# Optimization experiments

Hardware: AMD Instinct MI355X
Metric: run time of the kernel (lower is better)

The kernel has to match this reference:

```python
import jax, jax.numpy as jnp
import numpy as np


def setup_inputs() -> dict:
    key = jax.random.key(0)
    ks = jax.random.split(key, 5)
    B, S, D = 2, 2048, 1024
    x = jax.random.normal(ks[0], (B, S, D), dtype=jnp.float32)
    # nn.Linear default init scale ~ 1/sqrt(fan_in); use scaled normals
    W_qkv = jax.random.normal(ks[1], (3 * D, D), dtype=jnp.float32) * (1.0 / np.sqrt(D))
    b_qkv = jax.random.normal(ks[2], (3 * D,), dtype=jnp.float32) * 0.01
    W_out = jax.random.normal(ks[3], (D, D), dtype=jnp.float32) * (1.0 / np.sqrt(D))
    b_out = jax.random.normal(ks[4], (D,), dtype=jnp.float32) * 0.01
    return {"x": x, "W_qkv": W_qkv, "b_qkv": b_qkv, "W_out": W_out, "b_out": b_out, "n_heads": 16}


def reference(x, W_qkv, b_qkv, W_out, b_out, n_heads):
    B, S, D = x.shape
    H = n_heads
    c = D // H
    scale = jnp.asarray(1.0 / np.sqrt(c), dtype=x.dtype)
    # qkv projection; torch layout: (head, qkv, c) along the 3*D output dim
    qkv = (x @ W_qkv.T + b_qkv).reshape(B, S, H, 3, c)
    q = qkv[..., 0, :]  # (B, S, H, c)
    k = qkv[..., 1, :]
    v = qkv[..., 2, :]
    scores = jnp.einsum("bshd,bthd->bhst", q, k) * scale  # (B, H, S, S)
    # mask='right': forbid attending to future positions (col > row)
    causal = jnp.arange(S)[None, :] > jnp.arange(S)[:, None]  # (S, S) True where future
    scores = jnp.where(causal[None, None], -jnp.inf, scores)
    attn = jax.nn.softmax(scores, axis=-1)
    ctx = jnp.einsum("bhst,bthd->bshd", attn, v).reshape(B, S, D)
    return ctx @ W_out.T + b_out
```

## Files before the change

kernel.cpp:

```cpp
#include <hip/hip_runtime.h>
#include <stdint.h>

#define B_ 2
#define S_ 2048
#define D_ 1024
#define H_ 16
#define C_ 64
#define M_ (B_*S_)
#define N1_ (3*D_)

typedef float f32x4 __attribute__((ext_vector_type(4)));
typedef float f32x16 __attribute__((ext_vector_type(16)));
typedef __bf16 bf16x8 __attribute__((ext_vector_type(8)));

#define QSCALE 0.18033688f

static __device__ __forceinline__ unsigned short f2bf(float f) {
  __bf16 h = (__bf16)f;
  return __builtin_bit_cast(unsigned short, h);
}
static __device__ __forceinline__ unsigned pk2(float lo, float hi) {
  return (unsigned)f2bf(lo) | ((unsigned)f2bf(hi) << 16);
}

static __device__ __forceinline__ f32x4 mfma_bf16(uint4 a, uint4 b, f32x4 c) {
  return __builtin_amdgcn_mfma_f32_16x16x32_bf16(
      __builtin_bit_cast(bf16x8, a), __builtin_bit_cast(bf16x8, b), c, 0, 0, 0);
}
static __device__ __forceinline__ f32x16 mfma32(uint4 a, uint4 b, f32x16 c) {
  return __builtin_amdgcn_mfma_f32_32x32x16_bf16(
      __builtin_bit_cast(bf16x8, a), __builtin_bit_cast(bf16x8, b), c, 0, 0, 0);
}

static __device__ __forceinline__ float xsum32(float x) {
  return x + __shfl_xor(x, 32);
}

static __device__ __forceinline__ void gload16(const void* g, void* l) {
  __builtin_amdgcn_global_load_lds(
      (const __attribute__((address_space(1))) unsigned int*)g,
      (__attribute__((address_space(3))) unsigned int*)l, 16, 0, 0);
}

#define N8X (M_*D_/8)
#define N8W (N1_*D_/8)
#define N8O (D_*D_/8)
__global__ __launch_bounds__(256) void cast_all(
    const float* __restrict__ x,   unsigned short* __restrict__ xb,
    const float* __restrict__ wq,  unsigned short* __restrict__ wqb,
    const float* __restrict__ wo,  unsigned short* __restrict__ wob) {
  int i = blockIdx.x * 256 + threadIdx.x;
  const float* src; unsigned short* dst; int j;
  if (i < N8X)              { src = x;  dst = xb;  j = i; }
  else if (i < N8X + N8W)   { src = wq; dst = wqb; j = i - N8X; }
  else                      { src = wo; dst = wob; j = i - N8X - N8W; }
  const float4* s4 = (const float4*)src;
  float4 a = s4[2*j], b = s4[2*j+1];
  uint4 o;
  o.x = pk2(a.x, a.y);
  o.y = pk2(a.z, a.w);
  o.z = pk2(b.x, b.y);
  o.w = pk2(b.z, b.w);
  ((uint4*)dst)[j] = o;
}

template<int MODE>
__global__ __launch_bounds__(256) void gemm_bt(
    const unsigned short* __restrict__ A,
    const unsigned short* __restrict__ Bm,
    const float* __restrict__ bias,
    float* __restrict__ Cf,
    unsigned short* __restrict__ Qg,
    unsigned short* __restrict__ Kf,
    unsigned short* __restrict__ Vf,
    int Ndim, int Kdim)
{
  __shared__ __attribute__((aligned(16))) unsigned short As[128*32];
  __shared__ __attribute__((aligned(16))) unsigned short Bs[128*32];
  const int tid = threadIdx.x;
  const int l = tid & 63, wid = tid >> 6;
  const int g = l >> 4, lr = l & 15;
  const int m0 = blockIdx.y * 128, n0 = blockIdx.x * 128;
  const int wr = (wid >> 1) * 64, wc = (wid & 1) * 64;

  f32x4 acc[4][4] = {};

  const int lane4 = l >> 2;
  const int p4 = l & 3;
  const int cA = p4 ^ (lane4 & 3);
  const int rA = wid*32 + lane4;
  const unsigned short* Agl = A + (size_t)(m0 + rA) * Kdim + cA*8;
  const unsigned short* Bgl = Bm + (size_t)(n0 + rA) * Kdim + cA*8;
  unsigned short* Al0 = &As[(wid*32)*32];
  unsigned short* Al1 = &As[(wid*32+16)*32];
  unsigned short* Bl0 = &Bs[(wid*32)*32];
  unsigned short* Bl1 = &Bs[(wid*32+16)*32];
  const size_t rowstep = (size_t)16 * Kdim;

  for (int k0 = 0; k0 < Kdim; k0 += 32) {
    __syncthreads();
    gload16(Agl + k0,           Al0);
    gload16(Agl + k0 + rowstep, Al1);
    gload16(Bgl + k0,           Bl0);
    gload16(Bgl + k0 + rowstep, Bl1);
    __syncthreads();
    uint4 af[4], bf[4];
#pragma unroll
    for (int mi = 0; mi < 4; ++mi)
      af[mi] = *(const uint4*)&As[(wr + mi*16 + lr)*32 + ((g ^ (lr & 3))*8)];
#pragma unroll
    for (int ni = 0; ni < 4; ++ni)
      bf[ni] = *(const uint4*)&Bs[(wc + ni*16 + lr)*32 + ((g ^ (lr & 3))*8)];
#pragma unroll
    for (int mi = 0; mi < 4; ++mi)
#pragma unroll
      for (int ni = 0; ni < 4; ++ni)
        acc[mi][ni] = mfma_bf16(af[mi], bf[ni], acc[mi][ni]);
  }

#pragma unroll
  for (int mi = 0; mi < 4; ++mi)
#pragma unroll
    for (int ni = 0; ni < 4; ++ni) {
      if (MODE == 0) {
#pragma unroll
        for (int r = 0; r < 4; ++r) {
          const int row = m0 + wr + mi*16 + g*4 + r;
          const int col = n0 + wc + ni*16 + lr;
          Cf[(size_t)row * Ndim + col] = acc[mi][ni][r] + bias[col];
        }
      } else {
        const int colbase = n0 + wc + ni*16;
        const int h     = colbase / 192;
        const int rem   = colbase % 192;
        const int which = rem >> 6;
        const int cb    = rem & 63;
        const float bv  = bias[colbase + lr];
        const int row0  = m0 + wr + mi*16 + g*4;
        const int b     = row0 >> 11, s0 = row0 & 2047;
        const size_t bh32 = (size_t)(b*H_ + h) * 32;
        if (which == 0) {
#pragma unroll
          for (int r = 0; r < 4; ++r) {
            const float v = (acc[mi][ni][r] + bv) * QSCALE;
            Qg[((size_t)(b*H_ + h)*S_ + (s0 + r))*C_ + cb + lr] = f2bf(v);
          }
        } else if (which == 1) {
          const int kc = cb >> 4, hi = lr >> 3, j = lr & 7;
          const int kvb = s0 >> 6, kq = s0 & 63;
          const int half = kq >> 5, qlb = kq & 31;
          const size_t base = (((bh32 + kvb)*2 + half)*4 + kc)*512 + hi*256 + j;
#pragma unroll
          for (int r = 0; r < 4; ++r)
            Kf[base + (size_t)(qlb + r)*8] = f2bf(acc[mi][ni][r] + bv);
        } else {
          const int d = cb + lr;
          const int dhalf = d >> 5, ql = d & 31;
          const int kvb = s0 >> 6, kq = s0 & 63;
          const int kc = kq >> 4, hi = (kq >> 3) & 1, j0 = kq & 7;
          const size_t base = (((bh32 + kvb)*2 + dhalf)*4 + kc)*512
                              + (hi*32 + ql)*8 + j0;
          ushort4 pk;
          pk.x = f2bf(acc[mi][ni][0] + bv);
          pk.y = f2bf(acc[mi][ni][1] + bv);
          pk.z = f2bf(acc[mi][ni][2] + bv);
          pk.w = f2bf(acc[mi][ni][3] + bv);
          *(ushort4*)(Vf + base) = pk;
        }
      }
    }
}

#define PS_ 72
__global__ __launch_bounds__(256) void attn_fwd(
    const unsigned short* __restrict__ Qg,
    const unsigned short* __restrict__ Kf,
    const unsigned short* __restrict__ Vf,
    unsigned short* __restrict__ ctx)
{
  __shared__ __attribute__((aligned(16))) unsigned short Ps[4][32*PS_];

  const int tid = threadIdx.x, l = tid & 63, w = tid >> 6;
  const int ql = l & 31, hi = l >> 5;
  const int bh = blockIdx.x;
  const int y = (int)blockIdx.y;
  const int qtab[4] = {y, 63 - y, 31 - y, 32 + y};
  const int qt = qtab[w];
  const int qw0 = qt * 32;
  const int qg = qw0 + ql;
  const size_t baseK = (size_t)bh * S_ * C_;

  uint4 qreg[4];
  {
    const unsigned short* qp = Qg + baseK + (size_t)qg * C_ + hi * 8;
#pragma unroll
    for (int kc = 0; kc < 4; ++kc) qreg[kc] = *(const uint4*)(qp + 16*kc);
  }

  f32x16 acc0 = {}, acc1 = {};
  float lsum = 0.f;

  const unsigned short* pK = Kf + (size_t)bh * (32*4096) + (size_t)l * 8;
  const unsigned short* pV = Vf + (size_t)bh * (32*4096) + (size_t)l * 8;
  unsigned short* Pw = Ps[w];

  const int myend = qw0 + 32;
  for (int kv0 = 0; kv0 < myend; kv0 += 64) {
    const size_t kb = (size_t)(kv0 >> 6) * 4096;

    uint4 kf0[4], kf1[4];
#pragma unroll
    for (int kc = 0; kc < 4; ++kc) {
      kf0[kc] = *(const uint4*)(pK + kb + kc*512);
      kf1[kc] = *(const uint4*)(pK + kb + 2048 + kc*512);
    }
    f32x16 st0 = {}, st1 = {};
    __builtin_amdgcn_s_setprio(1);
#pragma unroll
    for (int kc = 0; kc < 4; ++kc) {
      st0 = mfma32(kf0[kc], qreg[kc], st0);
      st1 = mfma32(kf1[kc], qreg[kc], st1);
    }
    __builtin_amdgcn_s_setprio(0);

    uint4 vf0[4], vf1[4];
#pragma unroll
    for (int kc = 0; kc < 4; ++kc) {
      vf0[kc] = *(const uint4*)(pV + kb + kc*512);
      vf1[kc] = *(const uint4*)(pV + kb + 2048 + kc*512);
    }

    if (kv0 + 63 > qw0) {
#pragma unroll
      for (int r = 0; r < 16; ++r) {
        const int krow = (r & 3) + 8*(r >> 2) + 4*hi;
        if (kv0 + krow      > qg) st0[r] = -1e30f;
        if (kv0 + 32 + krow > qg) st1[r] = -1e30f;
      }
    }

    float ps[8];
#pragma unroll
    for (int j = 0; j < 8; ++j) {
      st0[2*j]   = exp2f(st0[2*j]);
      st0[2*j+1] = exp2f(st0[2*j+1]);
      st1[2*j]   = exp2f(st1[2*j]);
      st1[2*j+1] = exp2f(st1[2*j+1]);
      ps[j] = (st0[2*j] + st0[2*j+1]) + (st1[2*j] + st1[2*j+1]);
    }
    ps[0] += ps[4]; ps[1] += ps[5]; ps[2] += ps[6]; ps[3] += ps[7];
    lsum += (ps[0] + ps[1]) + (ps[2] + ps[3]);

#pragma unroll
    for (int r = 0; r < 16; r += 4) {
      const int k0i = (r >> 2)*8 + 4*hi;
      uint2 a0, a1;
      a0.x = pk2(st0[r],   st0[r+1]);  a0.y = pk2(st0[r+2], st0[r+3]);
      a1.x = pk2(st1[r],   st1[r+1]);  a1.y = pk2(st1[r+2], st1[r+3]);
      *(uint2*)&Pw[ql*PS_ + k0i]      = a0;
      *(uint2*)&Pw[ql*PS_ + 32 + k0i] = a1;
    }
    uint4 pb[4];
#pragma unroll
    for (int kc = 0; kc < 4; ++kc)
      pb[kc] = *(const uint4*)&Pw[ql*PS_ + kc*16 + hi*8];

    __builtin_amdgcn_s_setprio(1);
#pragma unroll
    for (int kc = 0; kc < 4; ++kc) {
      acc0 = mfma32(vf0[kc], pb[kc], acc0);
      acc1 = mfma32(vf1[kc], pb[kc], acc1);
    }
    __builtin_amdgcn_s_setprio(0);
  }

  const float inv = 1.0f / xsum32(lsum);
#pragma unroll
  for (int r = 0; r < 16; ++r) {
    const int d0 = (r & 3) + 8*(r >> 2) + 4*hi;
    Pw[ql*PS_ + ( d0       ^ (8*(ql & 7)))] = f2bf(acc0[r] * inv);
    Pw[ql*PS_ + ((32 + d0) ^ (8*(ql & 7)))] = f2bf(acc1[r] * inv);
  }
  const int q1 = l >> 1, half = l & 1;
  const unsigned short* Er = Pw + q1*PS_;
  const int b = bh >> 4, h = bh & 15;
  unsigned short* outp = ctx + ((size_t)(b*S_ + qw0 + q1))*D_ + h*C_;
#pragma unroll
  for (int j = 0; j < 4; ++j) {
    const int clog = half*4 + j;
    const int cx = clog ^ (q1 & 7);
    uint4 val = *(const uint4*)&Er[cx*8];
    *(uint4*)(outp + clog*8) = val;
  }
}

extern "C" void kernel_launch(void* const* d_in, const int* in_sizes, int n_in,
                              void* d_out, int out_size, void* d_ws, size_t ws_size,
                              hipStream_t stream) {
  const float* x    = (const float*)d_in[0];
  const float* Wqkv = (const float*)d_in[1];
  const float* bqkv = (const float*)d_in[2];
  const float* Wout = (const float*)d_in[3];
  const float* bout = (const float*)d_in[4];
  float* out = (float*)d_out;

  unsigned short* ws = (unsigned short*)d_ws;
  unsigned short* xb    = ws;
  unsigned short* wqkvb = xb    + (size_t)M_ * D_;
  unsigned short* woutb = wqkvb + (size_t)N1_ * D_;
  unsigned short* Qb    = woutb + (size_t)D_ * D_;
  unsigned short* Kfb   = Qb    + (size_t)B_*H_*S_*C_;
  unsigned short* Vfb   = Kfb   + (size_t)B_*H_*S_*C_;
  unsigned short* ctxb  = Vfb   + (size_t)B_*H_*S_*C_;

  {
    const int ntot = N8X + N8W + N8O;
    cast_all<<<dim3((ntot+255)/256), dim3(256), 0, stream>>>(
        x, xb, Wqkv, wqkvb, Wout, woutb);
  }

  gemm_bt<1><<<dim3(N1_/128, M_/128), dim3(256), 0, stream>>>(
      xb, wqkvb, bqkv, nullptr, Qb, Kfb, Vfb, N1_, D_);

  attn_fwd<<<dim3(32, 16), dim3(256), 0, stream>>>(Qb, Kfb, Vfb, ctxb);

  gemm_bt<0><<<dim3(D_/128, M_/128), dim3(256), 0, stream>>>(
      ctxb, woutb, bout, out, nullptr, nullptr, nullptr, D_, D_);
}
```

Measured before the change: 132.6 us.

## Split KV range across waves within a block and reduce partial attention results in LDS

Previously each of the four waves in a block owned its own 32-row query tile, with tiles paired to balance causal work, and walked the whole KV range alone. Now each block owns a single query tile, and its four waves take interleaved 64-wide KV chunks. The waves then combine their partial context accumulators and row sums through a two-step tree reduction in shared memory. The grid grows to four times as many blocks, launched heaviest tiles first, to shorten each wave's serial KV loop and improve latency hiding. The cost is extra barriers and shared-memory traffic for the reduction, and idle waves on short causal tiles.

```diff
diff --git a/kernel.cpp b/kernel.cpp
--- a/kernel.cpp
+++ b/kernel.cpp
@@ -179,13 +179,13 @@
     unsigned short* __restrict__ ctx)
 {
   __shared__ __attribute__((aligned(16))) unsigned short Ps[4][32*PS_];
+  float* Cmb0 = (float*)&Ps[0][0];
+  float* Cmb1 = Cmb0 + 2112;
 
   const int tid = threadIdx.x, l = tid & 63, w = tid >> 6;
   const int ql = l & 31, hi = l >> 5;
   const int bh = blockIdx.x;
-  const int y = (int)blockIdx.y;
-  const int qtab[4] = {y, 63 - y, 31 - y, 32 + y};
-  const int qt = qtab[w];
+  const int qt = 63 - (int)blockIdx.y;
   const int qw0 = qt * 32;
   const int qg = qw0 + ql;
   const size_t baseK = (size_t)bh * S_ * C_;
@@ -204,9 +204,10 @@
   const unsigned short* pV = Vf + (size_t)bh * (32*4096) + (size_t)l * 8;
   unsigned short* Pw = Ps[w];
 
-  const int myend = qw0 + 32;
-  for (int kv0 = 0; kv0 < myend; kv0 += 64) {
-    const size_t kb = (size_t)(kv0 >> 6) * 4096;
+  const int n_t = (qt + 2) >> 1;
+  for (int i = w; i < n_t; i += 4) {
+    const int kv0 = i * 64;
+    const size_t kb = (size_t)i * 4096;
 
     uint4 kf0[4], kf1[4];
 #pragma unroll
@@ -272,6 +273,52 @@
       acc1 = mfma32(vf1[kc], pb[kc], acc1);
     }
     __builtin_amdgcn_s_setprio(0);
+  }
+
+  __syncthreads();
+  if (w >= 2) {
+    float* Cb = (w == 2) ? Cmb0 : Cmb1;
+#pragma unroll
+    for (int r = 0; r < 16; ++r) {
+      const int d0 = (r & 3) + 8*(r >> 2) + 4*hi;
+      Cb[d0*32 + ql]        = acc0[r];
+      Cb[(d0 + 32)*32 + ql] = acc1[r];
+    }
+    Cb[2048 + l] = lsum;
+  }
+  __syncthreads();
+  if (w < 2) {
+    const float* Cb = (w == 0) ? Cmb0 : Cmb1;
+#pragma unroll
+    for (int r = 0; r < 16; ++r) {
+      const int d0 = (r & 3) + 8*(r >> 2) + 4*hi;
+      acc0[r] += Cb[d0*32 + ql];
+      acc1[r] += Cb[(d0 + 32)*32 + ql];
+    }
+    lsum += Cb[2048 + l];
+  }
+  __syncthreads();
+  if (w == 1) {
+    float* Cb = Cmb0;
+#pragma unroll
+    for (int r = 0; r < 16; ++r) {
+      const int d0 = (r & 3) + 8*(r >> 2) + 4*hi;
+      Cb[d0*32 + ql]        = acc0[r];
+      Cb[(d0 + 32)*32 + ql] = acc1[r];
+    }
+    Cb[2048 + l] = lsum;
+  }
+  __syncthreads();
+  if (w != 0) return;
+  {
+    const float* Cb = Cmb0;
+#pragma unroll
+    for (int r = 0; r < 16; ++r) {
+      const int d0 = (r & 3) + 8*(r >> 2) + 4*hi;
+      acc0[r] += Cb[d0*32 + ql];
+      acc1[r] += Cb[(d0 + 32)*32 + ql];
+    }
+    lsum += Cb[2048 + l];
   }
 
   const float inv = 1.0f / xsum32(lsum);
@@ -322,7 +369,7 @@
   gemm_bt<1><<<dim3(N1_/128, M_/128), dim3(256), 0, stream>>>(
       xb, wqkvb, bqkv, nullptr, Qb, Kfb, Vfb, N1_, D_);
 
-  attn_fwd<<<dim3(32, 16), dim3(256), 0, stream>>>(Qb, Kfb, Vfb, ctxb);
+  attn_fwd<<<dim3(32, 64), dim3(256), 0, stream>>>(Qb, Kfb, Vfb, ctxb);
 
   gemm_bt<0><<<dim3(D_/128, M_/128), dim3(256), 0, stream>>>(
       ctxb, woutb, bout, out, nullptr, nullptr, nullptr, D_, D_);
```

Result: faster. 126.9 us (-4.3%).
